# Performance work log

Hardware: AMD Instinct MI355X
Metric: run time of the kernel (lower is better)

Reference implementation:

```python
import jax, jax.numpy as jnp
import numpy as np

# dims: B batch, N tokens (64x64 grid), D slot/feature dim, H heads, HD head_dim
B, N, D = 32, 4096, 256
H, HD = 4, 64            # H * HD == qkv_size == D
S = 16                   # num slots
GH = 128                 # grid-encoder MLP hidden size
MH = 1024                # slot MLP hidden size
NUM_ITER = 3
EPS = 1e-8               # module epsilon
LN_EPS = 1e-6            # flax LayerNorm default


def _ln(x, s, b):
    m = jnp.mean(x, -1, keepdims=True)
    v = jnp.mean(jnp.square(x - m), -1, keepdims=True)
    return (x - m) * jax.lax.rsqrt(v + LN_EPS) * s + b


def setup_inputs() -> dict:
    key = jax.random.key(0)
    ks = jax.random.split(key, 16)
    g = lambda i, shape, scale: jax.random.normal(ks[i], shape, jnp.float32) * scale
    return {
        "slots": g(0, (B, S, D), 1.0),
        "inputs": g(1, (B, N, D + 2), 1.0),  # last 2 channels = coordinate grid
        "ln_in_s": jnp.ones((D,), jnp.float32), "ln_in_b": jnp.zeros((D,), jnp.float32),
        "Wk": g(2, (D, H, HD), D ** -0.5),
        "Wv": g(3, (D, H, HD), D ** -0.5),
        "Wp": g(4, (2, H, HD), 0.5),
        "ge_ln_s": jnp.ones((HD,), jnp.float32), "ge_ln_b": jnp.zeros((HD,), jnp.float32),
        "ge_W1": g(5, (HD, GH), HD ** -0.5), "ge_b1": jnp.zeros((GH,), jnp.float32),
        "ge_W2": g(6, (GH, HD), GH ** -0.5), "ge_b2": jnp.zeros((HD,), jnp.float32),
        "lnq_s": jnp.ones((D,), jnp.float32), "lnq_b": jnp.zeros((D,), jnp.float32),
        "Wq": g(7, (D, H, HD), D ** -0.5),
        "Wo": g(8, (H, HD, D), D ** -0.5),
        "gru_Wi": g(9, (D, 3 * D), D ** -0.5), "gru_bi": jnp.zeros((3 * D,), jnp.float32),
        "gru_Wh": g(10, (D, 3 * D), D ** -0.5), "gru_bhn": jnp.zeros((D,), jnp.float32),
        "mlp_ln_s": jnp.ones((D,), jnp.float32), "mlp_ln_b": jnp.zeros((D,), jnp.float32),
        "mlp_W1": g(11, (D, MH), D ** -0.5), "mlp_b1": jnp.zeros((MH,), jnp.float32),
        "mlp_W2": g(12, (MH, D), MH ** -0.5), "mlp_b2": jnp.zeros((D,), jnp.float32),
    }


def reference(slots, inputs, ln_in_s, ln_in_b, Wk, Wv, Wp, ge_ln_s, ge_ln_b,
              ge_W1, ge_b1, ge_W2, ge_b2, lnq_s, lnq_b, Wq, Wo,
              gru_Wi, gru_bi, gru_Wh, gru_bhn,
              mlp_ln_s, mlp_ln_b, mlp_W1, mlp_b1, mlp_W2, mlp_b2):
    feats, grid = inputs[..., :-2], inputs[..., -2:]
    x = _ln(feats, ln_in_s, ln_in_b)                         # [B,N,D] input pre-norm

    def grid_enc(y):                                          # MLP, pre-LN, no residual
        h = _ln(y, ge_ln_s, ge_ln_b)
        h = jax.nn.relu(h @ ge_W1 + ge_b1)
        return h @ ge_W2 + ge_b2

    p = jnp.einsum('bng,ghe->bnhe', grid, Wp)                 # grid projector
    k = grid_enc(jnp.einsum('bnd,dhe->bnhe', x, Wk) + p)      # [B,N,H,HD]
    v = grid_enc(jnp.einsum('bnd,dhe->bnhe', x, Wv) + p)      # [B,N,H,HD]

    scale = HD ** -0.5
    for _ in range(NUM_ITER):
        sn = _ln(slots, lnq_s, lnq_b)
        q = jnp.einsum('bsd,dhe->bshe', sn, Wq) * scale       # [B,S,H,HD]
        attn = jnp.einsum('bqhe,bkhe->bhqk', q, k)            # [B,H,S,N]
        attn = jax.nn.softmax(attn, axis=-2)                  # inverted: over slots
        attn = attn / (jnp.sum(attn, -1, keepdims=True) + EPS)  # renormalize over keys
        upd = jnp.einsum('bhqk,bkhe->bqhe', attn, v)          # [B,S,H,HD]
        upd = jnp.einsum('bqhe,hed->bqd', upd, Wo)            # multi-head merge -> [B,S,D]
        # flax GRUCell: hidden = slots, input = upd
        gi = upd @ gru_Wi + gru_bi
        gh = slots @ gru_Wh
        ir, iz, inn = jnp.split(gi, 3, -1)
        hr, hz, hn = jnp.split(gh, 3, -1)
        r = jax.nn.sigmoid(ir + hr)
        z = jax.nn.sigmoid(iz + hz)
        n = jnp.tanh(inn + r * (hn + gru_bhn))
        slots = (1.0 - z) * n + z * slots
        # residual pre-LN MLP
        h = _ln(slots, mlp_ln_s, mlp_ln_b)
        h = jax.nn.relu(h @ mlp_W1 + mlp_b1) @ mlp_W2 + mlp_b2
        slots = slots + h
    return slots
```

## Files before the change

### kernel.cpp

```cpp
#include <hip/hip_runtime.h>

using u16 = unsigned short;
using u32 = unsigned int;

#define Bn 32
#define Nn 4096
#define Dn 256
#define Hn 4
#define HDn 64
#define Sn 16

typedef __bf16 bf16x8 __attribute__((ext_vector_type(8)));
typedef float  f32x4  __attribute__((ext_vector_type(4)));

#define MFMA16(a,b,c) __builtin_amdgcn_mfma_f32_16x16x32_bf16((a),(b),(c),0,0,0)
#define CFENCE() __asm__ __volatile__("" ::: "memory")

__device__ __forceinline__ float bf2f(u16 u){ u32 x=((u32)u)<<16; float f; __builtin_memcpy(&f,&x,4); return f; }
__device__ __forceinline__ u16 f2bf(float f){ __bf16 h=(__bf16)f; u16 u; __builtin_memcpy(&u,&h,2); return u; }
__device__ __forceinline__ u32 pack2(float a,float b){ return (u32)f2bf(a)|((u32)f2bf(b)<<16); }
__device__ __forceinline__ float sigm(float x){ x=fminf(fmaxf(x,-30.f),30.f); return 1.f/(1.f+__expf(-x)); }
__device__ __forceinline__ float tanhfast(float x){ x=fminf(fmaxf(x,-15.f),15.f); float t=__expf(-2.f*x); return (1.f-t)/(1.f+t); }
__device__ __forceinline__ float gld(const void* p, int idx, bool f32){
  return f32 ? ((const float*)p)[idx] : bf2f(((const u16*)p)[idx]);
}
__device__ __forceinline__ bool is_f32(const u32* flagw){ return *flagw == 0x3F800000u; }

#define PB_LNS 0
#define PB_LNB 256
#define PB_WP 512
#define PB_GES 1024
#define PB_GEB 1088
#define PB_GB1 1152
#define PB_GB2 1280
#define PB_LQS 1344
#define PB_LQB 1600
#define PB_GBI 1856
#define PB_GBHN 2624
#define PB_MLS 2880
#define PB_MLB 3136
#define PB_MB1 3392
#define PB_MB2 4416
#define PB_TOT 4672

__global__ __launch_bounds__(256) void k_prep(
  const void* __restrict__ Wk, const void* __restrict__ Wv,
  const void* __restrict__ gW1, const void* __restrict__ gW2,
  const void* __restrict__ Wq, const void* __restrict__ Wo,
  const void* __restrict__ Wi, const void* __restrict__ Wh,
  const void* __restrict__ mW1, const void* __restrict__ mW2,
  const void* __restrict__ slots_in,
  const void* __restrict__ ln_s, const void* __restrict__ ln_b, const void* __restrict__ Wp,
  const void* __restrict__ ge_s, const void* __restrict__ ge_b,
  const void* __restrict__ geb1, const void* __restrict__ geb2,
  const void* __restrict__ lnqs, const void* __restrict__ lnqb,
  const void* __restrict__ gbi, const void* __restrict__ gbhn,
  const void* __restrict__ mls, const void* __restrict__ mlb,
  const void* __restrict__ mb1, const void* __restrict__ mb2,
  u16* __restrict__ Wcat_t, u16* __restrict__ Wq_t, u16* __restrict__ W1t,
  u16* __restrict__ W2t, u16* __restrict__ Wo_t, u16* __restrict__ Wi_t,
  u16* __restrict__ Wh_t, u16* __restrict__ mW1t, u16* __restrict__ mW2t,
  float* __restrict__ slots_cur, float* __restrict__ pb)
{
  bool f32 = is_f32((const u32*)ln_s);
  int idx = blockIdx.x*256 + threadIdx.x;
  if (idx < 65536){ int o=idx>>8,d=idx&255; Wcat_t[idx]=f2bf(gld(Wk,d*256+o,f32)); return; } idx-=65536;
  if (idx < 65536){ int o=idx>>8,d=idx&255; Wcat_t[65536+idx]=f2bf(gld(Wv,d*256+o,f32)); return; } idx-=65536;
  if (idx < 8192){ int n=idx>>6,k=idx&63; W1t[idx]=f2bf(gld(gW1,k*128+n,f32)); return; } idx-=8192;
  if (idx < 8192){ int n=idx>>7,k=idx&127; W2t[idx]=f2bf(gld(gW2,k*64+n,f32)); return; } idx-=8192;
  if (idx < 65536){ int o=idx>>8,d=idx&255; Wq_t[idx]=f2bf(gld(Wq,d*256+o,f32)); return; } idx-=65536;
  if (idx < 65536){ int d=idx>>8,he=idx&255; Wo_t[idx]=f2bf(gld(Wo,he*256+d,f32)); return; } idx-=65536;
  if (idx < 196608){ int n=idx>>8,k=idx&255; Wi_t[idx]=f2bf(gld(Wi,k*768+n,f32)); return; } idx-=196608;
  if (idx < 196608){ int n=idx>>8,k=idx&255; Wh_t[idx]=f2bf(gld(Wh,k*768+n,f32)); return; } idx-=196608;
  if (idx < 262144){ int n=idx>>8,k=idx&255; mW1t[idx]=f2bf(gld(mW1,k*1024+n,f32)); return; } idx-=262144;
  if (idx < 262144){ int n=idx>>10,k=idx&1023; mW2t[idx]=f2bf(gld(mW2,k*256+n,f32)); return; } idx-=262144;
  if (idx < 131072){ slots_cur[idx]=gld(slots_in,idx,f32); return; } idx-=131072;
  if (idx < 256){ pb[PB_LNS+idx]=gld(ln_s,idx,f32); return; } idx-=256;
  if (idx < 256){ pb[PB_LNB+idx]=gld(ln_b,idx,f32); return; } idx-=256;
  if (idx < 512){ pb[PB_WP+idx]=gld(Wp,idx,f32); return; } idx-=512;
  if (idx < 64){ pb[PB_GES+idx]=gld(ge_s,idx,f32); return; } idx-=64;
  if (idx < 64){ pb[PB_GEB+idx]=gld(ge_b,idx,f32); return; } idx-=64;
  if (idx < 128){ pb[PB_GB1+idx]=gld(geb1,idx,f32); return; } idx-=128;
  if (idx < 64){ pb[PB_GB2+idx]=gld(geb2,idx,f32); return; } idx-=64;
  if (idx < 256){ pb[PB_LQS+idx]=gld(lnqs,idx,f32); return; } idx-=256;
  if (idx < 256){ pb[PB_LQB+idx]=gld(lnqb,idx,f32); return; } idx-=256;
  if (idx < 768){ pb[PB_GBI+idx]=gld(gbi,idx,f32); return; } idx-=768;
  if (idx < 256){ pb[PB_GBHN+idx]=gld(gbhn,idx,f32); return; } idx-=256;
  if (idx < 256){ pb[PB_MLS+idx]=gld(mls,idx,f32); return; } idx-=256;
  if (idx < 256){ pb[PB_MLB+idx]=gld(mlb,idx,f32); return; } idx-=256;
  if (idx < 1024){ pb[PB_MB1+idx]=gld(mb1,idx,f32); return; } idx-=1024;
  if (idx < 256){ pb[PB_MB2+idx]=gld(mb2,idx,f32); return; }
}

__global__ __launch_bounds__(256, 3) void k_feat(
  const void* __restrict__ inputs, const u32* __restrict__ flagw,
  const float* __restrict__ pb,
  const u16* __restrict__ Wcat_t, const u16* __restrict__ W1t_g, const u16* __restrict__ W2t_g,
  u16* __restrict__ Kb, u16* __restrict__ Vb)
{
  __shared__ __align__(16) char sm[53248];
  u16* x_lds = (u16*)sm;
  float* misc = (float*)(sm + 16896);
  float* lnS = misc;      float* lnB = misc+256;
  float* wp0 = misc+512;  float* wp1 = misc+768;
  float* geS = misc+1024; float* geB = misc+1088;
  float* gB1 = misc+1152; float* gB2 = misc+1280;
  float* gxy = misc+1344;

  int tid = threadIdx.x;
  int batch = blockIdx.x >> 7;
  int n0 = (blockIdx.x & 127) << 5;
  bool f32 = is_f32(flagw);

  lnS[tid]=pb[PB_LNS+tid]; lnB[tid]=pb[PB_LNB+tid];
  wp0[tid]=pb[PB_WP+tid];  wp1[tid]=pb[PB_WP+256+tid];
  if (tid < 64){ geS[tid]=pb[PB_GES+tid]; geB[tid]=pb[PB_GEB+tid]; gB2[tid]=pb[PB_GB2+tid]; }
  if (tid < 128) gB1[tid]=pb[PB_GB1+tid];
  __syncthreads();

  {
    int row = tid>>3, seg = tid&7;
    size_t rowbase = ((size_t)(batch*Nn + n0 + row))*258;
    float v[32]; float sum=0.f, ssq=0.f;
    if (f32){
      const float2* ip = (const float2*)((const float*)inputs + rowbase + seg*32);
      #pragma unroll
      for (int i=0;i<16;i++){ float2 t=ip[i]; v[2*i]=t.x; v[2*i+1]=t.y; sum+=t.x+t.y; ssq+=t.x*t.x+t.y*t.y; }
      if (seg==0){
        const float* gp = (const float*)inputs + rowbase + 256;
        gxy[row*2]=gp[0]; gxy[row*2+1]=gp[1];
      }
    } else {
      const u32* ip = (const u32*)inputs + ((rowbase + seg*32)>>1);
      #pragma unroll
      for (int i=0;i<16;i++){ u32 u=ip[i]; float a=bf2f((u16)(u&0xffff)), b=bf2f((u16)(u>>16));
        v[2*i]=a; v[2*i+1]=b; sum+=a+b; ssq+=a*a+b*b; }
      if (seg==0){
        u32 u = *((const u32*)inputs + ((rowbase + 256)>>1));
        gxy[row*2]=bf2f((u16)(u&0xffff)); gxy[row*2+1]=bf2f((u16)(u>>16));
      }
    }
    sum += __shfl_xor(sum,1); sum += __shfl_xor(sum,2); sum += __shfl_xor(sum,4);
    ssq += __shfl_xor(ssq,1); ssq += __shfl_xor(ssq,2); ssq += __shfl_xor(ssq,4);
    float m = sum*(1.f/256.f);
    float var = ssq*(1.f/256.f) - m*m;
    float rs = rsqrtf(var + 1e-6f);
    u32* xw = (u32*)(x_lds + row*264 + seg*32);
    #pragma unroll
    for (int i=0;i<16;i++){
      int c = seg*32 + 2*i;
      float a=(v[2*i]-m)*rs*lnS[c]+lnB[c];
      float b=(v[2*i+1]-m)*rs*lnS[c+1]+lnB[c+1];
      xw[i]=pack2(a,b);
    }
  }
  __syncthreads();

  int wv = tid>>6, lane = tid&63, quad = lane>>4, l15 = lane&15;
  int h = wv;
  u16* bufA = (u16*)(sm + 22528 + wv*7680);
  u16* bufB = (u16*)(sm + 22528 + wv*7680 + 5120);

  float g0[2], g1[2];
  g0[0]=gxy[l15*2];      g1[0]=gxy[l15*2+1];
  g0[1]=gxy[(16+l15)*2]; g1[1]=gxy[(16+l15)*2+1];

  for (int pass=0; pass<2; pass++){
    f32x4 acc[4][2];
    #pragma unroll
    for (int mi=0;mi<4;mi++){ acc[mi][0]=(f32x4){0,0,0,0}; acc[mi][1]=(f32x4){0,0,0,0}; }
    const u16* Wb = Wcat_t + pass*65536;
    #pragma unroll
    for (int ks=0; ks<8; ks++){
      bf16x8 bx[2];
      #pragma unroll
      for (int nt=0;nt<2;nt++) bx[nt] = *(const bf16x8*)(x_lds + (nt*16+l15)*264 + ks*32 + quad*8);
      #pragma unroll
      for (int mi=0;mi<4;mi++){
        bf16x8 aw = *(const bf16x8*)(Wb + (h*64+mi*16+l15)*256 + ks*32 + quad*8);
        acc[mi][0] = MFMA16(aw, bx[0], acc[mi][0]);
        acc[mi][1] = MFMA16(aw, bx[1], acc[mi][1]);
      }
    }
    float vv[4][2][4];
    float s0=0.f, s1=0.f, q0s=0.f, q1s=0.f;
    #pragma unroll
    for (int mi=0;mi<4;mi++)
      #pragma unroll
      for (int r=0;r<4;r++){
        int eg = h*64 + mi*16 + quad*4 + r;
        float w0 = wp0[eg], w1 = wp1[eg];
        float a = acc[mi][0][r] + g0[0]*w0 + g1[0]*w1;
        float b = acc[mi][1][r] + g0[1]*w0 + g1[1]*w1;
        vv[mi][0][r]=a; vv[mi][1][r]=b;
        s0+=a; q0s+=a*a; s1+=b; q1s+=b*b;
      }
    s0 += __shfl_xor(s0,16); s0 += __shfl_xor(s0,32);
    s1 += __shfl_xor(s1,16); s1 += __shfl_xor(s1,32);
    q0s += __shfl_xor(q0s,16); q0s += __shfl_xor(q0s,32);
    q1s += __shfl_xor(q1s,16); q1s += __shfl_xor(q1s,32);
    float m0 = s0*(1.f/64.f), m1 = s1*(1.f/64.f);
    float rs0 = rsqrtf(q0s*(1.f/64.f) - m0*m0 + 1e-6f);
    float rs1 = rsqrtf(q1s*(1.f/64.f) - m1*m1 + 1e-6f);
    CFENCE();
    #pragma unroll
    for (int mi=0;mi<4;mi++)
      #pragma unroll
      for (int rp=0;rp<2;rp++){
        int el0 = mi*16 + quad*4 + 2*rp;
        float ga = geS[el0], gb_ = geB[el0], gc = geS[el0+1], gd = geB[el0+1];
        u32 wA = pack2((vv[mi][0][2*rp]-m0)*rs0*ga+gb_, (vv[mi][0][2*rp+1]-m0)*rs0*gc+gd);
        u32 wB = pack2((vv[mi][1][2*rp]-m1)*rs1*ga+gb_, (vv[mi][1][2*rp+1]-m1)*rs1*gc+gd);
        *(u32*)(bufA + (l15)*72 + el0)      = wA;
        *(u32*)(bufA + (16+l15)*72 + el0)   = wB;
      }
    CFENCE();
    f32x4 acc2[4][2];
    #pragma unroll
    for (int mi=0;mi<4;mi++){ acc2[mi][0]=(f32x4){0,0,0,0}; acc2[mi][1]=(f32x4){0,0,0,0}; }
    for (int qq=0; qq<4; qq++){
      f32x4 a1[2][2];
      #pragma unroll
      for (int ml=0;ml<2;ml++){ a1[ml][0]=(f32x4){0,0,0,0}; a1[ml][1]=(f32x4){0,0,0,0}; }
      #pragma unroll
      for (int ks2=0; ks2<2; ks2++){
        bf16x8 bh[2];
        #pragma unroll
        for (int nt=0;nt<2;nt++) bh[nt] = *(const bf16x8*)(bufA + (nt*16+l15)*72 + ks2*32 + quad*8);
        #pragma unroll
        for (int ml=0;ml<2;ml++){
          bf16x8 aW = *(const bf16x8*)(W1t_g + ((qq*2+ml)*16+l15)*64 + ks2*32 + quad*8);
          a1[ml][0] = MFMA16(aW, bh[0], a1[ml][0]);
          a1[ml][1] = MFMA16(aW, bh[1], a1[ml][1]);
        }
      }
      CFENCE();
      #pragma unroll
      for (int ml=0;ml<2;ml++)
        #pragma unroll
        for (int rp=0;rp<2;rp++){
          int ghl = ml*16 + quad*4 + 2*rp;
          float b1a = gB1[qq*32+ghl], b1b = gB1[qq*32+ghl+1];
          u32 wA = pack2(fmaxf(a1[ml][0][2*rp]+b1a,0.f), fmaxf(a1[ml][0][2*rp+1]+b1b,0.f));
          u32 wB = pack2(fmaxf(a1[ml][1][2*rp]+b1a,0.f), fmaxf(a1[ml][1][2*rp+1]+b1b,0.f));
          *(u32*)(bufB + (l15)*40 + ghl)    = wA;
          *(u32*)(bufB + (16+l15)*40 + ghl) = wB;
        }
      CFENCE();
      bf16x8 bq[2];
      #pragma unroll
      for (int nt=0;nt<2;nt++) bq[nt] = *(const bf16x8*)(bufB + (nt*16+l15)*40 + quad*8);
      #pragma unroll
      for (int mi=0;mi<4;mi++){
        bf16x8 a2 = *(const bf16x8*)(W2t_g + (mi*16+l15)*128 + qq*32 + quad*8);
        acc2[mi][0] = MFMA16(a2, bq[0], acc2[mi][0]);
        acc2[mi][1] = MFMA16(a2, bq[1], acc2[mi][1]);
      }
    }
    CFENCE();
    if (pass==0){
      #pragma unroll
      for (int mi=0;mi<4;mi++)
        #pragma unroll
        for (int rp=0;rp<2;rp++){
          int el0 = mi*16 + quad*4 + 2*rp;
          float b2a = gB2[el0], b2b = gB2[el0+1];
          u32 wA = pack2(acc2[mi][0][2*rp]+b2a, acc2[mi][0][2*rp+1]+b2b);
          u32 wB = pack2(acc2[mi][1][2*rp]+b2a, acc2[mi][1][2*rp+1]+b2b);
          *(u32*)(bufA + (l15)*72 + el0)    = wA;
          *(u32*)(bufA + (16+l15)*72 + el0) = wB;
        }
      CFENCE();
      int row = lane>>1, half = lane&1;
      uint4 t0 = *(const uint4*)(bufA + row*72 + half*32);
      uint4 t1 = *(const uint4*)(bufA + row*72 + half*32 + 8);
      uint4 t2 = *(const uint4*)(bufA + row*72 + half*32 + 16);
      uint4 t3 = *(const uint4*)(bufA + row*72 + half*32 + 24);
      u16* dst = Kb + ((size_t)((batch*Hn+h)*Nn + n0 + row))*64 + half*32;
      ((uint4*)dst)[0]=t0; ((uint4*)dst)[1]=t1;
      u16* dst2 = dst + 16;
      ((uint4*)(dst2))[0]=t2; ((uint4*)(dst2))[1]=t3;
    } else {
      #pragma unroll
      for (int mi=0;mi<4;mi++)
        #pragma unroll
        for (int r=0;r<4;r++){
          int e2 = mi*16 + quad*4 + r;
          float b2 = gB2[e2];
          bufA[e2*40 + l15]      = f2bf(acc2[mi][0][r]+b2);
          bufA[e2*40 + 16 + l15] = f2bf(acc2[mi][1][r]+b2);
        }
      CFENCE();
      int e = lane;
      uint4 t0 = *(const uint4*)(bufA + e*40);
      uint4 t1 = *(const uint4*)(bufA + e*40 + 8);
      uint4 t2 = *(const uint4*)(bufA + e*40 + 16);
      uint4 t3 = *(const uint4*)(bufA + e*40 + 24);
      u16* dst = Vb + ((size_t)((batch*Hn+h)*HDn + e))*Nn + n0;
      ((uint4*)dst)[0]=t0; ((uint4*)dst)[1]=t1; ((uint4*)dst)[2]=t2; ((uint4*)dst)[3]=t3;
    }
    CFENCE();
  }
}

__global__ __launch_bounds__(256) void k_attn(
  const float* __restrict__ slots_cur, const float* __restrict__ pb,
  const u16* __restrict__ Wq_t, const u16* __restrict__ Kb, const u16* __restrict__ Vb,
  float* __restrict__ num_part, float* __restrict__ den_part)
{
  __shared__ u16 sn[16*264];
  __shared__ u16 qld[16*72];
  __shared__ u16 pld[4][16*40];
  int tid = threadIdx.x;
  int chunk = blockIdx.x, h = blockIdx.y, b = blockIdx.z;

  {
    int rowq = tid>>4, li = tid&15;
    const float* sp = slots_cur + ((size_t)(b*16+rowq))*256 + li*16;
    float v[16]; float sum=0.f, ssq=0.f;
    #pragma unroll
    for (int i=0;i<16;i++){ float x=sp[i]; v[i]=x; sum+=x; ssq+=x*x; }
    sum += __shfl_xor(sum,1); sum += __shfl_xor(sum,2); sum += __shfl_xor(sum,4); sum += __shfl_xor(sum,8);
    ssq += __shfl_xor(ssq,1); ssq += __shfl_xor(ssq,2); ssq += __shfl_xor(ssq,4); ssq += __shfl_xor(ssq,8);
    float m = sum*(1.f/256.f);
    float var = ssq*(1.f/256.f) - m*m;
    float rs = rsqrtf(var + 1e-6f);
    u32* dst = (u32*)(sn + rowq*264 + li*16);
    #pragma unroll
    for (int i=0;i<8;i++){
      int c = li*16 + 2*i;
      float a=(v[2*i]-m)*rs*pb[PB_LQS+c]+pb[PB_LQB+c];
      float bval=(v[2*i+1]-m)*rs*pb[PB_LQS+c+1]+pb[PB_LQB+c+1];
      dst[i]=pack2(a,bval);
    }
  }
  __syncthreads();

  int wv = tid>>6, lane = tid&63, quad = lane>>4, l15 = lane&15;
  {
    f32x4 qa = (f32x4){0,0,0,0};
    #pragma unroll
    for (int ks=0; ks<8; ks++){
      bf16x8 a = *(const bf16x8*)(sn + l15*264 + ks*32 + quad*8);
      bf16x8 bb = *(const bf16x8*)(Wq_t + (h*64 + wv*16 + l15)*256 + ks*32 + quad*8);
      qa = MFMA16(a, bb, qa);
    }
    #pragma unroll
    for (int r=0;r<4;r++) qld[(quad*4+r)*72 + wv*16 + l15] = f2bf(qa[r]*0.125f);
  }
  __syncthreads();

  bf16x8 qb0 = *(const bf16x8*)(qld + l15*72 + quad*8);
  bf16x8 qb1 = *(const bf16x8*)(qld + l15*72 + 32 + quad*8);
  f32x4 vacc[4];
  #pragma unroll
  for (int nt=0;nt<4;nt++) vacc[nt]=(f32x4){0,0,0,0};
  float denp = 0.f;
  const u16* Kbase = Kb + ((size_t)(b*Hn+h))*Nn*64;
  const u16* Vbase = Vb + ((size_t)(b*Hn+h))*64*Nn;
  u16* myp = pld[wv];

  for (int it=0; it<8; it++){
    int g0 = chunk*1024 + wv*256 + it*32;
    float pn[2][4];
    #pragma unroll
    for (int s=0;s<2;s++){
      bf16x8 a0 = *(const bf16x8*)(Kbase + (size_t)(g0+s*16+l15)*64 + quad*8);
      bf16x8 a1 = *(const bf16x8*)(Kbase + (size_t)(g0+s*16+l15)*64 + 32 + quad*8);
      f32x4 c = (f32x4){0,0,0,0};
      c = MFMA16(a0, qb0, c);
      c = MFMA16(a1, qb1, c);
      #pragma unroll
      for (int r=0;r<4;r++){
        float sc = c[r];
        float mx = sc;
        mx = fmaxf(mx, __shfl_xor(mx,1)); mx = fmaxf(mx, __shfl_xor(mx,2));
        mx = fmaxf(mx, __shfl_xor(mx,4)); mx = fmaxf(mx, __shfl_xor(mx,8));
        float e = __expf(sc - mx);
        float t = e;
        t += __shfl_xor(t,1); t += __shfl_xor(t,2); t += __shfl_xor(t,4); t += __shfl_xor(t,8);
        float p = e / t;
        float pr = bf2f(f2bf(p));
        pn[s][r] = p; denp += pr;
      }
    }
    CFENCE();
    #pragma unroll
    for (int s=0;s<2;s++){
      uint2 w; w.x = pack2(pn[s][0], pn[s][1]); w.y = pack2(pn[s][2], pn[s][3]);
      *(uint2*)(myp + l15*40 + s*16 + quad*4) = w;
    }
    CFENCE();
    bf16x8 pa = *(const bf16x8*)(myp + l15*40 + quad*8);
    #pragma unroll
    for (int nt=0;nt<4;nt++){
      bf16x8 vb = *(const bf16x8*)(Vbase + (size_t)(nt*16+l15)*Nn + g0 + quad*8);
      vacc[nt] = MFMA16(pa, vb, vacc[nt]);
    }
  }
  denp += __shfl_xor(denp,16); denp += __shfl_xor(denp,32);
  int wc = chunk*4 + wv;
  float* np = num_part + ((size_t)((b*Hn+h)*16 + wc))*1024;
  #pragma unroll
  for (int nt=0;nt<4;nt++)
    #pragma unroll
    for (int r=0;r<4;r++) np[(quad*4+r)*64 + nt*16 + l15] = vacc[nt][r];
  if (lane < 16) den_part[((b*Hn+h)*16 + wc)*16 + lane] = denp;
}

__global__ __launch_bounds__(256) void k_slot(
  float* __restrict__ slots_cur, const float* __restrict__ num_part, const float* __restrict__ den_part,
  const u16* __restrict__ Wo_t, const u16* __restrict__ Wi_t, const u16* __restrict__ Wh_t,
  const u16* __restrict__ mW1t, const u16* __restrict__ mW2t,
  const float* __restrict__ pb, const u32* __restrict__ flagw,
  void* __restrict__ out)
{
  __shared__ __align__(16) char sm[59392];
  u16* upd_b    = (u16*)(sm);
  u16* updo_b   = (u16*)(sm+8448);
  float* slots_f= (float*)(sm+16896);
  u16* hr_b     = (u16*)(sm);
  u16* slhm_b   = (u16*)(sm+33792);
  float* snew_f = (float*)(sm+42240);
  float* den_l  = (float*)(sm+59136);
  int tid = threadIdx.x, b = blockIdx.x;
  bool of32 = is_f32(flagw);

  {
    const float* sp = slots_cur + (size_t)b*4096;
    for (int i=tid; i<4096; i+=256){
      int sl=i>>8, c=i&255; float v=sp[i];
      slots_f[sl*264+c]=v; slhm_b[sl*264+c]=f2bf(v);
    }
  }
  if (tid < 64){
    int h=tid>>4, sl=tid&15; float s=0.f;
    for (int wc=0; wc<16; wc++) s += den_part[((b*Hn+h)*16+wc)*16 + sl];
    den_l[tid] = s + 1e-8f;
  }
  __syncthreads();
  {
    int he = tid, h = he>>6, e = he&63;
    for (int sl=0; sl<16; sl++){
      float s=0.f;
      for (int wc=0; wc<16; wc++)
        s += num_part[((size_t)((b*Hn+h)*16+wc))*1024 + sl*64 + e];
      upd_b[sl*264 + he] = f2bf(s / den_l[h*16+sl]);
    }
  }
  __syncthreads();

  int wv = tid>>6, lane = tid&63, quad = lane>>4, l15 = lane&15;
  {
    f32x4 acc[4];
    #pragma unroll
    for (int j=0;j<4;j++) acc[j]=(f32x4){0,0,0,0};
    #pragma unroll
    for (int ks=0; ks<8; ks++){
      bf16x8 a = *(const bf16x8*)(upd_b + l15*264 + ks*32 + quad*8);
      #pragma unroll
      for (int j=0;j<4;j++){
        bf16x8 bb = *(const bf16x8*)(Wo_t + ((wv*4+j)*16+l15)*256 + ks*32 + quad*8);
        acc[j] = MFMA16(a, bb, acc[j]);
      }
    }
    #pragma unroll
    for (int j=0;j<4;j++)
      #pragma unroll
      for (int r=0;r<4;r++) updo_b[(quad*4+r)*264 + (wv*4+j)*16 + l15] = f2bf(acc[j][r]);
  }
  __syncthreads();
  {
    f32x4 gi[3][4], gh[3][4];
    #pragma unroll
    for (int g=0;g<3;g++)
      #pragma unroll
      for (int j=0;j<4;j++){ gi[g][j]=(f32x4){0,0,0,0}; gh[g][j]=(f32x4){0,0,0,0}; }
    #pragma unroll
    for (int ks=0; ks<8; ks++){
      bf16x8 au = *(const bf16x8*)(updo_b + l15*264 + ks*32 + quad*8);
      bf16x8 as = *(const bf16x8*)(slhm_b + l15*264 + ks*32 + quad*8);
      #pragma unroll
      for (int g=0;g<3;g++)
        #pragma unroll
        for (int j=0;j<4;j++){
          int colg = g*256 + (wv*4+j)*16 + l15;
          bf16x8 bi_ = *(const bf16x8*)(Wi_t + (size_t)colg*256 + ks*32 + quad*8);
          bf16x8 bh_ = *(const bf16x8*)(Wh_t + (size_t)colg*256 + ks*32 + quad*8);
          gi[g][j] = MFMA16(au, bi_, gi[g][j]);
          gh[g][j] = MFMA16(as, bh_, gh[g][j]);
        }
    }
    #pragma unroll
    for (int j=0;j<4;j++){
      int dcol = (wv*4+j)*16 + l15;
      float bir = pb[PB_GBI+dcol], biz = pb[PB_GBI+256+dcol], bin = pb[PB_GBI+512+dcol];
      float bhn = pb[PB_GBHN+dcol];
      #pragma unroll
      for (int r=0;r<4;r++){
        int sl = quad*4 + r;
        float ir = gi[0][j][r]+bir, iz = gi[1][j][r]+biz, inn = gi[2][j][r]+bin;
        float hrr = gh[0][j][r], hz = gh[1][j][r], hn = gh[2][j][r];
        float rg = sigm(ir + hrr);
        float z  = sigm(iz + hz);
        float nn = tanhfast(inn + rg*(hn + bhn));
        float old = slots_f[sl*264 + dcol];
        snew_f[sl*264 + dcol] = (1.f - z)*nn + z*old;
      }
    }
  }
  __syncthreads();
  {
    int sl = tid>>4, li = tid&15;
    float v[16]; float sum=0.f, ssq=0.f;
    #pragma unroll
    for (int i=0;i<16;i++){ float x=snew_f[sl*264 + li*16 + i]; v[i]=x; sum+=x; ssq+=x*x; }
    sum += __shfl_xor(sum,1); sum += __shfl_xor(sum,2); sum += __shfl_xor(sum,4); sum += __shfl_xor(sum,8);
    ssq += __shfl_xor(ssq,1); ssq += __shfl_xor(ssq,2); ssq += __shfl_xor(ssq,4); ssq += __shfl_xor(ssq,8);
    float m = sum*(1.f/256.f);
    float var = ssq*(1.f/256.f) - m*m;
    float rs = rsqrtf(var + 1e-6f);
    #pragma unroll
    for (int i=0;i<16;i++){
      int c = li*16 + i;
      slhm_b[sl*264+c] = f2bf((v[i]-m)*rs*pb[PB_MLS+c] + pb[PB_MLB+c]);
    }
  }
  __syncthreads();
  {
    f32x4 acc[16];
    #pragma unroll
    for (int j=0;j<16;j++) acc[j]=(f32x4){0,0,0,0};
    #pragma unroll
    for (int ks=0; ks<8; ks++){
      bf16x8 a = *(const bf16x8*)(slhm_b + l15*264 + ks*32 + quad*8);
      #pragma unroll
      for (int j=0;j<16;j++){
        int col = (wv*16+j)*16 + l15;
        bf16x8 bb = *(const bf16x8*)(mW1t + (size_t)col*256 + ks*32 + quad*8);
        acc[j] = MFMA16(a, bb, acc[j]);
      }
    }
    __syncthreads();
    #pragma unroll
    for (int j=0;j<16;j++){
      int col = (wv*16+j)*16 + l15;
      float b1 = pb[PB_MB1+col];
      #pragma unroll
      for (int r=0;r<4;r++) hr_b[(quad*4+r)*1032 + col] = f2bf(fmaxf(acc[j][r]+b1, 0.f));
    }
  }
  __syncthreads();
  {
    f32x4 acc[4];
    #pragma unroll
    for (int j=0;j<4;j++) acc[j]=(f32x4){0,0,0,0};
    #pragma unroll
    for (int ks=0; ks<32; ks++){
      bf16x8 a = *(const bf16x8*)(hr_b + l15*1032 + ks*32 + quad*8);
      #pragma unroll
      for (int j=0;j<4;j++){
        int col = (wv*4+j)*16 + l15;
        bf16x8 bb = *(const bf16x8*)(mW2t + (size_t)col*1024 + ks*32 + quad*8);
        acc[j] = MFMA16(a, bb, acc[j]);
      }
    }
    #pragma unroll
    for (int j=0;j<4;j++)
      #pragma unroll
      for (int r=0;r<4;r++){
        int col = (wv*4+j)*16 + l15;
        int sl = quad*4 + r;
        float res = snew_f[sl*264+col] + acc[j][r] + pb[PB_MB2+col];
        size_t oi = (size_t)b*4096 + sl*256 + col;
        slots_cur[oi] = res;
        if (of32) ((float*)out)[oi] = res;
        else      ((u16*)out)[oi] = f2bf(res);
      }
  }
}

extern "C" void kernel_launch(void* const* d_in, const int* in_sizes, int n_in,
                              void* d_out, int out_size, void* d_ws, size_t ws_size,
                              hipStream_t stream)
{
  const void* slots_in = d_in[0];
  const void* inputs   = d_in[1];
  const void* ln_in_s  = d_in[2];
  const void* ln_in_b  = d_in[3];
  const void* Wk       = d_in[4];
  const void* Wv       = d_in[5];
  const void* Wp       = d_in[6];
  const void* ge_ln_s  = d_in[7];
  const void* ge_ln_b  = d_in[8];
  const void* ge_W1    = d_in[9];
  const void* ge_b1    = d_in[10];
  const void* ge_W2    = d_in[11];
  const void* ge_b2    = d_in[12];
  const void* lnq_s    = d_in[13];
  const void* lnq_b    = d_in[14];
  const void* Wq       = d_in[15];
  const void* Wo       = d_in[16];
  const void* gru_Wi   = d_in[17];
  const void* gru_bi   = d_in[18];
  const void* gru_Wh   = d_in[19];
  const void* gru_bhn  = d_in[20];
  const void* mlp_ln_s = d_in[21];
  const void* mlp_ln_b = d_in[22];
  const void* mlp_W1   = d_in[23];
  const void* mlp_b1   = d_in[24];
  const void* mlp_W2   = d_in[25];
  const void* mlp_b2   = d_in[26];

  char* ws = (char*)d_ws;
  u16* Wcat_t = (u16*)(ws + 0);
  u16* Wq_t   = (u16*)(ws + 262144);
  u16* W1t    = (u16*)(ws + 393216);
  u16* W2t    = (u16*)(ws + 409600);
  u16* Wo_t   = (u16*)(ws + 425984);
  u16* Wi_t   = (u16*)(ws + 557056);
  u16* Wh_t   = (u16*)(ws + 950272);
  u16* mW1t   = (u16*)(ws + 1343488);
  u16* mW2t   = (u16*)(ws + 1867776);
  u16* Kb     = (u16*)(ws + 2392064);
  u16* Vb     = (u16*)(ws + 69500928);
  float* slots_cur = (float*)(ws + 136609792);
  float* num_part  = (float*)(ws + 137134080);
  float* den_part  = (float*)(ws + 145522688);
  float* pb        = (float*)(ws + 145653760);

  const u32* flagw = (const u32*)ln_in_s;

  k_prep<<<5203, 256, 0, stream>>>(Wk, Wv, ge_W1, ge_W2, Wq, Wo, gru_Wi, gru_Wh,
                                   mlp_W1, mlp_W2, slots_in,
                                   ln_in_s, ln_in_b, Wp, ge_ln_s, ge_ln_b, ge_b1, ge_b2,
                                   lnq_s, lnq_b, gru_bi, gru_bhn, mlp_ln_s, mlp_ln_b,
                                   mlp_b1, mlp_b2,
                                   Wcat_t, Wq_t, W1t, W2t, Wo_t, Wi_t, Wh_t, mW1t, mW2t,
                                   slots_cur, pb);

  k_feat<<<4096, 256, 0, stream>>>(inputs, flagw, pb, Wcat_t, W1t, W2t, Kb, Vb);

  for (int iter=0; iter<3; iter++){
    k_attn<<<dim3(4,4,32), 256, 0, stream>>>(slots_cur, pb, Wq_t, Kb, Vb,
                                             num_part, den_part);
    k_slot<<<32, 256, 0, stream>>>(slots_cur, num_part, den_part, Wo_t, Wi_t, Wh_t,
                                   mW1t, mW2t, pb, flagw, d_out);
  }
}
```

Baseline: 943.0 us.

## Store V row-major like K and transpose per tile in LDS inside attention

The encoder kernel now writes V in the same token-major [N,64] layout as K, which removes the separate transposed scatter path. The attention kernel loads each 32-token V tile with contiguous 16-byte reads before the softmax and transposes it through a per-wave LDS buffer to feed the MFMA. The aim is to replace strided global V reads with coalesced ones and to overlap the V load with the score computation. The cost is extra LDS traffic from many 32-bit scattered writes, which may cause bank conflicts, plus more LDS allocation that could lower occupancy.

```diff
diff --git a/kernel.cpp b/kernel.cpp
--- a/kernel.cpp
+++ b/kernel.cpp
@@ -258,46 +258,27 @@
       }
     }
     CFENCE();
-    if (pass==0){
-      #pragma unroll
-      for (int mi=0;mi<4;mi++)
-        #pragma unroll
-        for (int rp=0;rp<2;rp++){
-          int el0 = mi*16 + quad*4 + 2*rp;
-          float b2a = gB2[el0], b2b = gB2[el0+1];
-          u32 wA = pack2(acc2[mi][0][2*rp]+b2a, acc2[mi][0][2*rp+1]+b2b);
-          u32 wB = pack2(acc2[mi][1][2*rp]+b2a, acc2[mi][1][2*rp+1]+b2b);
-          *(u32*)(bufA + (l15)*72 + el0)    = wA;
-          *(u32*)(bufA + (16+l15)*72 + el0) = wB;
-        }
-      CFENCE();
+    #pragma unroll
+    for (int mi=0;mi<4;mi++)
+      #pragma unroll
+      for (int rp=0;rp<2;rp++){
+        int el0 = mi*16 + quad*4 + 2*rp;
+        float b2a = gB2[el0], b2b = gB2[el0+1];
+        u32 wA = pack2(acc2[mi][0][2*rp]+b2a, acc2[mi][0][2*rp+1]+b2b);
+        u32 wB = pack2(acc2[mi][1][2*rp]+b2a, acc2[mi][1][2*rp+1]+b2b);
+        *(u32*)(bufA + (l15)*72 + el0)    = wA;
+        *(u32*)(bufA + (16+l15)*72 + el0) = wB;
+      }
+    CFENCE();
+    {
+      u16* Base = (pass==0) ? Kb : Vb;
       int row = lane>>1, half = lane&1;
       uint4 t0 = *(const uint4*)(bufA + row*72 + half*32);
       uint4 t1 = *(const uint4*)(bufA + row*72 + half*32 + 8);
       uint4 t2 = *(const uint4*)(bufA + row*72 + half*32 + 16);
       uint4 t3 = *(const uint4*)(bufA + row*72 + half*32 + 24);
-      u16* dst = Kb + ((size_t)((batch*Hn+h)*Nn + n0 + row))*64 + half*32;
-      ((uint4*)dst)[0]=t0; ((uint4*)dst)[1]=t1;
-      u16* dst2 = dst + 16;
-      ((uint4*)(dst2))[0]=t2; ((uint4*)(dst2))[1]=t3;
-    } else {
-      #pragma unroll
-      for (int mi=0;mi<4;mi++)
-        #pragma unroll
-        for (int r=0;r<4;r++){
-          int e2 = mi*16 + quad*4 + r;
-          float b2 = gB2[e2];
-          bufA[e2*40 + l15]      = f2bf(acc2[mi][0][r]+b2);
-          bufA[e2*40 + 16 + l15] = f2bf(acc2[mi][1][r]+b2);
-        }
-      CFENCE();
-      int e = lane;
-      uint4 t0 = *(const uint4*)(bufA + e*40);
-      uint4 t1 = *(const uint4*)(bufA + e*40 + 8);
-      uint4 t2 = *(const uint4*)(bufA + e*40 + 16);
-      uint4 t3 = *(const uint4*)(bufA + e*40 + 24);
-      u16* dst = Vb + ((size_t)((batch*Hn+h)*HDn + e))*Nn + n0;
-      ((uint4*)dst)[0]=t0; ((uint4*)dst)[1]=t1; ((uint4*)dst)[2]=t2; ((uint4*)dst)[3]=t3;
+      uint4* dst = (uint4*)(Base + ((size_t)((batch*Hn+h)*Nn + n0 + row))*64 + half*32);
+      dst[0]=t0; dst[1]=t1; dst[2]=t2; dst[3]=t3;
     }
     CFENCE();
   }
@@ -311,6 +292,7 @@
   __shared__ u16 sn[16*264];
   __shared__ u16 qld[16*72];
   __shared__ u16 pld[4][16*40];
+  __shared__ u16 ldsT[4][64*40];
   int tid = threadIdx.x;
   int chunk = blockIdx.x, h = blockIdx.y, b = blockIdx.z;
 
@@ -357,11 +339,19 @@
   for (int nt=0;nt<4;nt++) vacc[nt]=(f32x4){0,0,0,0};
   float denp = 0.f;
   const u16* Kbase = Kb + ((size_t)(b*Hn+h))*Nn*64;
-  const u16* Vbase = Vb + ((size_t)(b*Hn+h))*64*Nn;
+  const u16* Vbase = Vb + ((size_t)(b*Hn+h))*Nn*64;
   u16* myp = pld[wv];
+  u16* myT = ldsT[wv];
+  int k2 = lane&15, eq = lane>>4;
 
   for (int it=0; it<8; it++){
     int g0 = chunk*1024 + wv*256 + it*32;
+    const u16* vr0 = Vbase + (size_t)(g0 + 2*k2)*64 + eq*16;
+    const u16* vr1 = vr0 + 64;
+    uint4 va0 = ((const uint4*)vr0)[0];
+    uint4 va1 = ((const uint4*)(vr0+8))[0];
+    uint4 vb0 = ((const uint4*)vr1)[0];
+    uint4 vb1 = ((const uint4*)(vr1+8))[0];
     float pn[2][4];
     #pragma unroll
     for (int s=0;s<2;s++){
@@ -385,6 +375,16 @@
       }
     }
     CFENCE();
+    {
+      u16 ea[16], eb[16];
+      __builtin_memcpy(ea,   &va0, 16); __builtin_memcpy(ea+8, &va1, 16);
+      __builtin_memcpy(eb,   &vb0, 16); __builtin_memcpy(eb+8, &vb1, 16);
+      #pragma unroll
+      for (int i=0;i<16;i++){
+        int e = eq*16 + i;
+        *(u32*)(myT + e*40 + 2*k2) = (u32)ea[i] | ((u32)eb[i]<<16);
+      }
+    }
     #pragma unroll
     for (int s=0;s<2;s++){
       uint2 w; w.x = pack2(pn[s][0], pn[s][1]); w.y = pack2(pn[s][2], pn[s][3]);
@@ -394,9 +394,10 @@
     bf16x8 pa = *(const bf16x8*)(myp + l15*40 + quad*8);
     #pragma unroll
     for (int nt=0;nt<4;nt++){
-      bf16x8 vb = *(const bf16x8*)(Vbase + (size_t)(nt*16+l15)*Nn + g0 + quad*8);
+      bf16x8 vb = *(const bf16x8*)(myT + (nt*16+l15)*40 + quad*8);
       vacc[nt] = MFMA16(pa, vb, vacc[nt]);
     }
+    CFENCE();
   }
   denp += __shfl_xor(denp,16); denp += __shfl_xor(denp,32);
   int wc = chunk*4 + wv;
```

Result: faster. 842.6 us (-10.6%).
